# Kernel tuning notes

Measured on AMD Instinct MI355X. Metric: run time of the kernel, lower is better.

The kernel has to match this reference:

```python
import jax, jax.numpy as jnp
import numpy as np

B, S, DIN, DQK, DV = 4, 4096, 1024, 64, 64


def setup_inputs() -> dict:
    key = jax.random.key(0)
    ks = jax.random.split(key, 10)
    inv = 1.0 / np.sqrt(DIN)
    return {
        "query": jax.random.normal(ks[0], (B, S, DIN), dtype=jnp.float32),
        "key": jax.random.normal(ks[1], (B, S, DIN), dtype=jnp.float32),
        "value": jax.random.normal(ks[2], (B, S, DIN), dtype=jnp.float32),
        "mask": jnp.ones((B, S, S), dtype=jnp.int32),
        "Wq": jax.random.uniform(ks[3], (DIN, DQK), jnp.float32, -inv, inv),
        "bq": jax.random.uniform(ks[4], (DQK,), jnp.float32, -inv, inv),
        "Wk": jax.random.uniform(ks[5], (DIN, DQK), jnp.float32, -inv, inv),
        "bk": jax.random.uniform(ks[6], (DQK,), jnp.float32, -inv, inv),
        "Wv": jax.random.uniform(ks[7], (DIN, DV), jnp.float32, -inv, inv),
        "bv": jax.random.uniform(ks[8], (DV,), jnp.float32, -inv, inv),
    }


def reference(query, key, value, mask, Wq, bq, Wk, bk, Wv, bv):
    q = jnp.einsum("bsd,de->bse", query, Wq) + bq  # [B,S,DQK]
    k = jnp.einsum("bsd,de->bse", key, Wk) + bk    # [B,S,DQK]
    v = jnp.einsum("bsd,de->bse", value, Wv) + bv  # [B,S,DV]
    # faithful nonstandard scale: sqrt(dim_qk + 1e-8)
    scale = jnp.sqrt(jnp.float32(q.shape[-1]) + 1e-8)
    scores = jnp.einsum("bqe,bke->bqk", q, k) / scale  # [B,S,S]
    scores = jnp.where(mask == 0, jnp.float32(-jnp.inf), scores)
    attn = jax.nn.softmax(scores, axis=-1)
    return jnp.einsum("bqk,bkv->bqv", attn, v)  # [B,S,DV]
```

## Files before the change

kernel.cpp:

```cpp
#include <hip/hip_runtime.h>

#define NB 4
#define NS 4096
#define NDIN 1024
#define ND 64

typedef __attribute__((ext_vector_type(4))) float f32x4;
typedef __attribute__((ext_vector_type(8))) short s16x8;
typedef __attribute__((ext_vector_type(4))) short s16x4;

__device__ __forceinline__ unsigned short f2bf(float f) {
  union { float f; unsigned u; } x; x.f = f;
  unsigned r = x.u + 0x7fffu + ((x.u >> 16) & 1u);
  return (unsigned short)(r >> 16);
}

__device__ __forceinline__ unsigned cvtpk(float lo, float hi) {
  unsigned r;
  asm("v_cvt_pk_bf16_f32 %0, %1, %2" : "=v"(r) : "v"(lo), "v"(hi));
  return r;
}

__device__ __forceinline__ void gload16(const void* g, void* l) {
  __builtin_amdgcn_global_load_lds(
      (const __attribute__((address_space(1))) void*)g,
      (__attribute__((address_space(3))) void*)l, 16, 0, 0);
}

__global__ __launch_bounds__(256) void prep_w_kernel(
    const float* __restrict__ Wq, const float* __restrict__ Wk,
    const float* __restrict__ Wv, unsigned short* __restrict__ wt) {
  int idx = blockIdx.x * 256 + threadIdx.x;
  int m = idx >> 16;
  int r = idx & 65535;
  int c = r >> 10;
  int k = r & 1023;
  const float* W = (m == 0) ? Wq : (m == 1) ? Wk : Wv;
  wt[idx] = f2bf(W[k * ND + c]);
}

__global__ __launch_bounds__(256, 3) void proj_kernel(
    const float* __restrict__ Xq, const float* __restrict__ Xk, const float* __restrict__ Xv,
    const float* __restrict__ bq, const float* __restrict__ bk, const float* __restrict__ bv,
    const unsigned short* __restrict__ wt_all,
    unsigned short* __restrict__ q_o, unsigned short* __restrict__ k_o,
    unsigned short* __restrict__ vt_o) {
  __shared__ float xsm[2][4096];
  __shared__ unsigned short wsm[2][4096];

  const int y = blockIdx.y;
  const float* __restrict__ X = (y == 0) ? Xq : (y == 1) ? Xk : Xv;
  const float* __restrict__ bias = (y == 0) ? bq : (y == 1) ? bk : bv;
  const char* __restrict__ wg = (const char*)(wt_all + y * (ND * NDIN));
  const int row0 = blockIdx.x * 64;
  const int tid = threadIdx.x;
  const int lane = tid & 63;
  const int w = tid >> 6;
  const int ql = lane & 15;
  const int grp = lane >> 4;
  const int swz = (ql & 7) << 4;

  int osrcX[4];
  #pragma unroll
  for (int j = 0; j < 4; ++j) {
    const int o = w * 4096 + j * 1024 + lane * 16;
    const int row = o >> 8, c = o & 255;
    osrcX[j] = row * 4096 + (c ^ ((row & 7) << 4));
  }
  int osrcW[2];
  #pragma unroll
  for (int j = 0; j < 2; ++j) {
    const int o = w * 2048 + j * 1024 + lane * 16;
    const int row = o >> 7, c = o & 127;
    osrcW[j] = row * 2048 + (c ^ ((row & 7) << 4));
  }

  const char* xg = (const char*)(X + (size_t)row0 * NDIN);
  auto stageX = [&](int kk, int buf) {
    const char* src = xg + kk * 256;
    char* dst = (char*)xsm + buf * 16384 + w * 4096;
    #pragma unroll
    for (int j = 0; j < 4; ++j) gload16(src + osrcX[j], dst + j * 1024);
  };
  auto stageW = [&](int kk, int buf) {
    const char* src = wg + kk * 128;
    char* dst = (char*)wsm + buf * 8192 + w * 2048;
    gload16(src + osrcW[0], dst);
    gload16(src + osrcW[1], dst + 1024);
  };

  const int fw0 = (grp * 16) ^ swz;
  const int fw1 = (grp * 16 + 64) ^ swz;

  f32x4 acc[4] = {};

  stageX(0, 0);
  stageW(0, 0);
  asm volatile("s_waitcnt vmcnt(0)" ::: "memory");
  __syncthreads();

  for (int kk = 0; kk < 16; ++kk) {
    const int cur = kk & 1;
    if (kk < 15) {
      stageX(kk + 1, cur ^ 1);
      stageW(kk + 1, cur ^ 1);
    }
    __builtin_amdgcn_sched_barrier(0);

    const char* xr = (const char*)xsm + cur * 16384 + (16 * w + ql) * 256;
    const char* wr = (const char*)wsm + cur * 8192;
    #pragma unroll
    for (int half = 0; half < 2; ++half) {
      const f32x4 a0 = *reinterpret_cast<const f32x4*>(
          xr + ((half * 128 + grp * 32) ^ swz));
      const f32x4 a1 = *reinterpret_cast<const f32x4*>(
          xr + ((half * 128 + grp * 32 + 16) ^ swz));
      union { s16x8 v; unsigned u[4]; } a;
      a.u[0] = cvtpk(a0[0], a0[1]);
      a.u[1] = cvtpk(a0[2], a0[3]);
      a.u[2] = cvtpk(a1[0], a1[1]);
      a.u[3] = cvtpk(a1[2], a1[3]);
      const int fw = half ? fw1 : fw0;
      #pragma unroll
      for (int nt = 0; nt < 4; ++nt) {
        const s16x8 bfr = *reinterpret_cast<const s16x8*>(wr + (ql + 16 * nt) * 128 + fw);
        acc[nt] = __builtin_amdgcn_mfma_f32_16x16x32_bf16(a.v, bfr, acc[nt], 0, 0, 0);
      }
    }

    asm volatile("s_waitcnt vmcnt(0)" ::: "memory");
    __syncthreads();
  }

  const int b = row0 >> 12;
  const int s0 = row0 & 4095;
  #pragma unroll
  for (int nt = 0; nt < 4; ++nt) {
    const int col = ql + 16 * nt;
    const float bia = bias[col];
    #pragma unroll
    for (int r = 0; r < 4; ++r) {
      const int rr = 16 * w + grp * 4 + r;
      const unsigned short h = f2bf(acc[nt][r] + bia);
      if (y == 0) {
        q_o[(size_t)(row0 + rr) * ND + col] = h;
      } else if (y == 1) {
        k_o[(size_t)(row0 + rr) * ND + col] = h;
      } else {
        vt_o[(size_t)b * ND * NS + (size_t)col * NS + (s0 + rr)] = h;
      }
    }
  }
}

__global__ __launch_bounds__(256, 3) void attn_kernel(
    const unsigned short* __restrict__ qm, const unsigned short* __restrict__ km,
    const unsigned short* __restrict__ vt, const int* __restrict__ mask,
    float* __restrict__ opart, float* __restrict__ ml) {
  __shared__ unsigned short ksm[2][4096];
  __shared__ unsigned short vsm[2][4096];
  __shared__ unsigned short psm[4096];

  const int bid = blockIdx.x;
  const int combo = bid & 15;
  const int qblk = bid >> 4;
  const int b = combo >> 2;
  const int split = combo & 3;
  const int q0 = qblk * 64;
  const int kv00 = split * 1024;

  const int tid = threadIdx.x;
  const int lane = tid & 63;
  const int w = tid >> 6;
  const int ql = lane & 15;
  const int grp = lane >> 4;

  const int swz = (ql & 7) << 4;
  const int fK0 = ql * 128 + ((grp * 16) ^ swz);
  const int fK1 = ql * 128 + ((grp * 16 + 64) ^ swz);

  int oK0, oK1, oV0, oV1;
  {
    const int o0 = w * 2048 + lane * 16;
    const int o1 = o0 + 1024;
    oK0 = o0 ^ (((o0 >> 7) & 7) << 4);
    oK1 = o1 ^ (((o1 >> 7) & 7) << 4);
    const int d0 = o0 >> 7, c0 = o0 & 127;
    const int d1 = o1 >> 7, c1 = o1 & 127;
    oV0 = d0 * 8192 + (c0 ^ ((d0 & 7) << 4));
    oV1 = d1 * 8192 + (c1 ^ ((d1 & 7) << 4));
  }

  const char* kg = (const char*)(km + (size_t)b * NS * ND + (size_t)kv00 * ND);
  const char* vg = (const char*)(vt + (size_t)b * ND * NS + kv00);
  char* const klds = (char*)&ksm[0][0] + w * 2048;
  char* const vlds = (char*)&vsm[0][0] + w * 2048;
  char* const pw = (char*)&psm[0] + w * 2048;

  const size_t qrow = (size_t)(b * NS + q0 + w * 16 + ql) * ND;
  const s16x8 qf0 = *reinterpret_cast<const s16x8*>(qm + qrow + grp * 8);
  const s16x8 qf1 = *reinterpret_cast<const s16x8*>(qm + qrow + 32 + grp * 8);

  const int* __restrict__ mrow =
      mask + (size_t)(b * NS + q0 + w * 16 + ql) * NS + kv00;

  f32x4 acc[4] = {};
  float m_i = -INFINITY;
  float l_i = 0.f;
  const float CSC = 0.18033688011112042f;
  const float THR = 11.54f;

  auto stage = [&](int t, int buf) {
    const char* kt = kg + (size_t)t * 8192;
    const char* vtb = vg + (size_t)t * 128;
    gload16(kt + oK0, klds + buf * 8192);
    gload16(kt + oK1, klds + buf * 8192 + 1024);
    gload16(vtb + oV0, vlds + buf * 8192);
    gload16(vtb + oV1, vlds + buf * 8192 + 1024);
  };

  int4 mc[2][4];

  stage(0, 0);
  {
    mc[0][0] = *reinterpret_cast<const int4*>(mrow + grp * 4);
    mc[0][1] = *reinterpret_cast<const int4*>(mrow + 16 + grp * 4);
    mc[0][2] = *reinterpret_cast<const int4*>(mrow + 32 + grp * 4);
    mc[0][3] = *reinterpret_cast<const int4*>(mrow + 48 + grp * 4);
  }
  asm volatile("s_waitcnt vmcnt(0)" ::: "memory");
  __syncthreads();

  for (int tt = 0; tt < 16; tt += 2) {
    #pragma unroll
    for (int ph = 0; ph < 2; ++ph) {
      const int t = tt + ph;
      const int cur = ph;

      if (t < 15) {
        stage(t + 1, cur ^ 1);
        const int* mn = mrow + (t + 1) * 64;
        mc[ph ^ 1][0] = *reinterpret_cast<const int4*>(mn + grp * 4);
        mc[ph ^ 1][1] = *reinterpret_cast<const int4*>(mn + 16 + grp * 4);
        mc[ph ^ 1][2] = *reinterpret_cast<const int4*>(mn + 32 + grp * 4);
        mc[ph ^ 1][3] = *reinterpret_cast<const int4*>(mn + 48 + grp * 4);
      }
      __builtin_amdgcn_sched_barrier(0);

      const char* kread = (const char*)&ksm[0][0] + cur * 8192;
      const char* vread = (const char*)&vsm[0][0] + cur * 8192;

      f32x4 s4[4];
      __builtin_amdgcn_s_setprio(1);
      #pragma unroll
      for (int mt = 0; mt < 4; ++mt) {
        const s16x8 kf0 = *reinterpret_cast<const s16x8*>(kread + mt * 2048 + fK0);
        const s16x8 kf1 = *reinterpret_cast<const s16x8*>(kread + mt * 2048 + fK1);
        f32x4 s = {0.f, 0.f, 0.f, 0.f};
        s = __builtin_amdgcn_mfma_f32_16x16x32_bf16(kf0, qf0, s, 0, 0, 0);
        s = __builtin_amdgcn_mfma_f32_16x16x32_bf16(kf1, qf1, s, 0, 0, 0);
        s4[mt] = s;
      }
      __builtin_amdgcn_s_setprio(0);

      float sc[16];
      #pragma unroll
      for (int mt = 0; mt < 4; ++mt) {
        const int4 m = mc[ph][mt];
        sc[4 * mt + 0] = (m.x != 0) ? s4[mt][0] * CSC : -1e30f;
        sc[4 * mt + 1] = (m.y != 0) ? s4[mt][1] * CSC : -1e30f;
        sc[4 * mt + 2] = (m.z != 0) ? s4[mt][2] * CSC : -1e30f;
        sc[4 * mt + 3] = (m.w != 0) ? s4[mt][3] * CSC : -1e30f;
      }

      float t0 = fmaxf(fmaxf(sc[0], sc[1]), fmaxf(sc[2], sc[3]));
      float t1 = fmaxf(fmaxf(sc[4], sc[5]), fmaxf(sc[6], sc[7]));
      float t2 = fmaxf(fmaxf(sc[8], sc[9]), fmaxf(sc[10], sc[11]));
      float t3 = fmaxf(fmaxf(sc[12], sc[13]), fmaxf(sc[14], sc[15]));
      float tm = fmaxf(fmaxf(t0, t1), fmaxf(t2, t3));
      tm = fmaxf(tm, __shfl_xor(tm, 16));
      tm = fmaxf(tm, __shfl_xor(tm, 32));
      if (!__all(tm <= m_i + THR)) {
        const float nm = fmaxf(m_i, tm);
        const float alpha = exp2f(m_i - nm);
        #pragma unroll
        for (int r = 0; r < 4; ++r) {
          const float ar = __shfl(alpha, grp * 4 + r);
          acc[0][r] *= ar;
          acc[1][r] *= ar;
          acc[2][r] *= ar;
          acc[3][r] *= ar;
        }
        l_i *= alpha;
        m_i = nm;
      }
      #pragma unroll
      for (int r = 0; r < 16; ++r) sc[r] = exp2f(sc[r] - m_i);
      float u0 = (sc[0] + sc[1]) + (sc[2] + sc[3]);
      float u1 = (sc[4] + sc[5]) + (sc[6] + sc[7]);
      float u2 = (sc[8] + sc[9]) + (sc[10] + sc[11]);
      float u3 = (sc[12] + sc[13]) + (sc[14] + sc[15]);
      float ssum = (u0 + u1) + (u2 + u3);
      ssum += __shfl_xor(ssum, 16);
      ssum += __shfl_xor(ssum, 32);
      l_i += ssum;

      #pragma unroll
      for (int mt = 0; mt < 4; ++mt) {
        uint2 pk;
        pk.x = cvtpk(sc[4 * mt + 0], sc[4 * mt + 1]);
        pk.y = cvtpk(sc[4 * mt + 2], sc[4 * mt + 3]);
        *reinterpret_cast<uint2*>(pw + ql * 128 + ((mt * 32 + grp * 8) ^ swz)) = pk;
      }

      #pragma unroll
      for (int ks = 0; ks < 2; ++ks) {
        const s16x8 pa = *reinterpret_cast<const s16x8*>(
            pw + ql * 128 + ((ks * 64 + grp * 16) ^ swz));
        const int fV = ks ? fK1 : fK0;
        __builtin_amdgcn_s_setprio(1);
        #pragma unroll
        for (int nt = 0; nt < 4; ++nt) {
          const s16x8 vb = *reinterpret_cast<const s16x8*>(vread + nt * 2048 + fV);
          acc[nt] = __builtin_amdgcn_mfma_f32_16x16x32_bf16(pa, vb, acc[nt], 0, 0, 0);
        }
        __builtin_amdgcn_s_setprio(0);
      }

      if (t < 15) {
        asm volatile("s_waitcnt vmcnt(16)" ::: "memory");
        __syncthreads();
      }
    }
  }

  const int qg = b * NS + q0 + w * 16;
  float* obase = opart + ((size_t)split * (NB * NS) + qg) * 64;
  #pragma unroll
  for (int nt = 0; nt < 4; ++nt) {
    #pragma unroll
    for (int r = 0; r < 4; ++r) {
      obase[(size_t)(grp * 4 + r) * 64 + ql + 16 * nt] = acc[nt][r];
    }
  }
  if (grp == 0) {
    float* mlp = ml + ((size_t)split * (NB * NS) + qg + ql) * 2;
    mlp[0] = m_i;
    mlp[1] = l_i;
  }
}

__global__ __launch_bounds__(256) void combine_kernel(
    const float* __restrict__ opart, const float* __restrict__ ml,
    float* __restrict__ out) {
  const int idx = blockIdx.x * 256 + threadIdx.x;
  const int q = idx >> 4;
  const int dc = (idx & 15) * 4;
  const float2 a0 = *reinterpret_cast<const float2*>(ml + (size_t)q * 2);
  const float2 a1 = *reinterpret_cast<const float2*>(ml + (size_t)(16384 + q) * 2);
  const float2 a2 = *reinterpret_cast<const float2*>(ml + (size_t)(32768 + q) * 2);
  const float2 a3 = *reinterpret_cast<const float2*>(ml + (size_t)(49152 + q) * 2);
  const float M = fmaxf(fmaxf(a0.x, a1.x), fmaxf(a2.x, a3.x));
  const float w0 = exp2f(a0.x - M), w1 = exp2f(a1.x - M);
  const float w2 = exp2f(a2.x - M), w3 = exp2f(a3.x - M);
  const float inv = 1.f / (a0.y * w0 + a1.y * w1 + a2.y * w2 + a3.y * w3);
  f32x4 o = (*reinterpret_cast<const f32x4*>(opart + (size_t)q * 64 + dc)) * w0;
  o += (*reinterpret_cast<const f32x4*>(opart + ((size_t)16384 + q) * 64 + dc)) * w1;
  o += (*reinterpret_cast<const f32x4*>(opart + ((size_t)32768 + q) * 64 + dc)) * w2;
  o += (*reinterpret_cast<const f32x4*>(opart + ((size_t)49152 + q) * 64 + dc)) * w3;
  o *= inv;
  *reinterpret_cast<f32x4*>(out + (size_t)q * 64 + dc) = o;
}

extern "C" void kernel_launch(void* const* d_in, const int* in_sizes, int n_in,
                              void* d_out, int out_size, void* d_ws, size_t ws_size,
                              hipStream_t stream) {
  const float* query = (const float*)d_in[0];
  const float* key   = (const float*)d_in[1];
  const float* value = (const float*)d_in[2];
  const int*   mask  = (const int*)d_in[3];
  const float* Wq = (const float*)d_in[4];
  const float* bq = (const float*)d_in[5];
  const float* Wk = (const float*)d_in[6];
  const float* bk = (const float*)d_in[7];
  const float* Wv = (const float*)d_in[8];
  const float* bv = (const float*)d_in[9];
  float* out = (float*)d_out;

  char* ws = (char*)d_ws;
  unsigned short* wt    = (unsigned short*)(ws);
  unsigned short* qb    = (unsigned short*)(ws + 393216);
  unsigned short* kb    = (unsigned short*)(ws + 2490368);
  unsigned short* vtb   = (unsigned short*)(ws + 4587520);
  float*          opart = (float*)(ws + 6684672);
  float*          mlb   = (float*)(ws + 23461888);

  prep_w_kernel<<<dim3(768), dim3(256), 0, stream>>>(Wq, Wk, Wv, wt);
  proj_kernel<<<dim3(256, 3), dim3(256), 0, stream>>>(query, key, value,
                                                      bq, bk, bv, wt, qb, kb, vtb);
  attn_kernel<<<dim3(1024), dim3(256), 0, stream>>>(qb, kb, vtb, mask, opart, mlb);
  combine_kernel<<<dim3(1024), dim3(256), 0, stream>>>(opart, mlb, out);
}
```

Before: 132.0 us.

## Drop split-KV and combine kernel; one block per query tile with XCD mapping

Removes the 4-way split over the key dimension, so each block walks all 4096 keys and normalizes its output directly, which eliminates the partial-output writes and the combine kernel launch. The grid shrinks from 1024 to 256 blocks, with block ids mapped so each XCD pair handles one batch for L2 locality. Launch bounds drop to one block per SM, and the barrier becomes a raw s_barrier. The risk is much less parallelism: 256 blocks on a 256-CU part gives one wave of long-running blocks, with less latency hiding for the large mask stream.

```diff
diff --git a/kernel.cpp b/kernel.cpp
--- a/kernel.cpp
+++ b/kernel.cpp
@@ -153,21 +153,19 @@
   }
 }
 
-__global__ __launch_bounds__(256, 3) void attn_kernel(
+__global__ __launch_bounds__(256, 1) void attn_kernel(
     const unsigned short* __restrict__ qm, const unsigned short* __restrict__ km,
     const unsigned short* __restrict__ vt, const int* __restrict__ mask,
-    float* __restrict__ opart, float* __restrict__ ml) {
+    float* __restrict__ out) {
   __shared__ unsigned short ksm[2][4096];
   __shared__ unsigned short vsm[2][4096];
   __shared__ unsigned short psm[4096];
 
   const int bid = blockIdx.x;
-  const int combo = bid & 15;
-  const int qblk = bid >> 4;
-  const int b = combo >> 2;
-  const int split = combo & 3;
+  const int xcd = bid & 7;
+  const int b = xcd >> 1;
+  const int qblk = (bid >> 3) + (xcd & 1) * 32;
   const int q0 = qblk * 64;
-  const int kv00 = split * 1024;
 
   const int tid = threadIdx.x;
   const int lane = tid & 63;
@@ -191,8 +189,8 @@
     oV1 = d1 * 8192 + (c1 ^ ((d1 & 7) << 4));
   }
 
-  const char* kg = (const char*)(km + (size_t)b * NS * ND + (size_t)kv00 * ND);
-  const char* vg = (const char*)(vt + (size_t)b * ND * NS + kv00);
+  const char* kg = (const char*)(km + (size_t)b * NS * ND);
+  const char* vg = (const char*)(vt + (size_t)b * ND * NS);
   char* const klds = (char*)&ksm[0][0] + w * 2048;
   char* const vlds = (char*)&vsm[0][0] + w * 2048;
   char* const pw = (char*)&psm[0] + w * 2048;
@@ -201,8 +199,7 @@
   const s16x8 qf0 = *reinterpret_cast<const s16x8*>(qm + qrow + grp * 8);
   const s16x8 qf1 = *reinterpret_cast<const s16x8*>(qm + qrow + 32 + grp * 8);
 
-  const int* __restrict__ mrow =
-      mask + (size_t)(b * NS + q0 + w * 16 + ql) * NS + kv00;
+  const int* __restrict__ mrow = mask + (size_t)(b * NS + q0 + w * 16 + ql) * NS;
 
   f32x4 acc[4] = {};
   float m_i = -INFINITY;
@@ -231,21 +228,22 @@
   asm volatile("s_waitcnt vmcnt(0)" ::: "memory");
   __syncthreads();
 
-  for (int tt = 0; tt < 16; tt += 2) {
+  for (int tt = 0; tt < 64; tt += 2) {
     #pragma unroll
     for (int ph = 0; ph < 2; ++ph) {
       const int t = tt + ph;
       const int cur = ph;
 
-      if (t < 15) {
+      if (t < 63) {
         stage(t + 1, cur ^ 1);
+        __builtin_amdgcn_sched_barrier(0);
         const int* mn = mrow + (t + 1) * 64;
         mc[ph ^ 1][0] = *reinterpret_cast<const int4*>(mn + grp * 4);
         mc[ph ^ 1][1] = *reinterpret_cast<const int4*>(mn + 16 + grp * 4);
         mc[ph ^ 1][2] = *reinterpret_cast<const int4*>(mn + 32 + grp * 4);
         mc[ph ^ 1][3] = *reinterpret_cast<const int4*>(mn + 48 + grp * 4);
-      }
-      __builtin_amdgcn_sched_barrier(0);
+        __builtin_amdgcn_sched_barrier(0);
+      }
 
       const char* kread = (const char*)&ksm[0][0] + cur * 8192;
       const char* vread = (const char*)&vsm[0][0] + cur * 8192;
@@ -327,49 +325,23 @@
         __builtin_amdgcn_s_setprio(0);
       }
 
-      if (t < 15) {
+      if (t < 63) {
         asm volatile("s_waitcnt vmcnt(16)" ::: "memory");
-        __syncthreads();
-      }
-    }
-  }
-
-  const int qg = b * NS + q0 + w * 16;
-  float* obase = opart + ((size_t)split * (NB * NS) + qg) * 64;
+        __builtin_amdgcn_s_barrier();
+      }
+    }
+  }
+
+  const float linv = 1.f / l_i;
+  float* obase = out + ((size_t)(b * NS + q0 + w * 16)) * 64;
   #pragma unroll
-  for (int nt = 0; nt < 4; ++nt) {
-    #pragma unroll
-    for (int r = 0; r < 4; ++r) {
-      obase[(size_t)(grp * 4 + r) * 64 + ql + 16 * nt] = acc[nt][r];
-    }
-  }
-  if (grp == 0) {
-    float* mlp = ml + ((size_t)split * (NB * NS) + qg + ql) * 2;
-    mlp[0] = m_i;
-    mlp[1] = l_i;
-  }
-}
-
-__global__ __launch_bounds__(256) void combine_kernel(
-    const float* __restrict__ opart, const float* __restrict__ ml,
-    float* __restrict__ out) {
-  const int idx = blockIdx.x * 256 + threadIdx.x;
-  const int q = idx >> 4;
-  const int dc = (idx & 15) * 4;
-  const float2 a0 = *reinterpret_cast<const float2*>(ml + (size_t)q * 2);
-  const float2 a1 = *reinterpret_cast<const float2*>(ml + (size_t)(16384 + q) * 2);
-  const float2 a2 = *reinterpret_cast<const float2*>(ml + (size_t)(32768 + q) * 2);
-  const float2 a3 = *reinterpret_cast<const float2*>(ml + (size_t)(49152 + q) * 2);
-  const float M = fmaxf(fmaxf(a0.x, a1.x), fmaxf(a2.x, a3.x));
-  const float w0 = exp2f(a0.x - M), w1 = exp2f(a1.x - M);
-  const float w2 = exp2f(a2.x - M), w3 = exp2f(a3.x - M);
-  const float inv = 1.f / (a0.y * w0 + a1.y * w1 + a2.y * w2 + a3.y * w3);
-  f32x4 o = (*reinterpret_cast<const f32x4*>(opart + (size_t)q * 64 + dc)) * w0;
-  o += (*reinterpret_cast<const f32x4*>(opart + ((size_t)16384 + q) * 64 + dc)) * w1;
-  o += (*reinterpret_cast<const f32x4*>(opart + ((size_t)32768 + q) * 64 + dc)) * w2;
-  o += (*reinterpret_cast<const f32x4*>(opart + ((size_t)49152 + q) * 64 + dc)) * w3;
-  o *= inv;
-  *reinterpret_cast<f32x4*>(out + (size_t)q * 64 + dc) = o;
+  for (int r = 0; r < 4; ++r) {
+    const float ar = __shfl(linv, grp * 4 + r);
+    #pragma unroll
+    for (int nt = 0; nt < 4; ++nt) {
+      obase[(size_t)(grp * 4 + r) * 64 + ql + 16 * nt] = acc[nt][r] * ar;
+    }
+  }
 }
 
 extern "C" void kernel_launch(void* const* d_in, const int* in_sizes, int n_in,
@@ -388,16 +360,13 @@
   float* out = (float*)d_out;
 
   char* ws = (char*)d_ws;
-  unsigned short* wt    = (unsigned short*)(ws);
-  unsigned short* qb    = (unsigned short*)(ws + 393216);
-  unsigned short* kb    = (unsigned short*)(ws + 2490368);
-  unsigned short* vtb   = (unsigned short*)(ws + 4587520);
-  float*          opart = (float*)(ws + 6684672);
-  float*          mlb   = (float*)(ws + 23461888);
+  unsigned short* wt  = (unsigned short*)(ws);
+  unsigned short* qb  = (unsigned short*)(ws + 393216);
+  unsigned short* kb  = (unsigned short*)(ws + 2490368);
+  unsigned short* vtb = (unsigned short*)(ws + 4587520);
 
   prep_w_kernel<<<dim3(768), dim3(256), 0, stream>>>(Wq, Wk, Wv, wt);
   proj_kernel<<<dim3(256, 3), dim3(256), 0, stream>>>(query, key, value,
                                                       bq, bk, bv, wt, qb, kb, vtb);
-  attn_kernel<<<dim3(1024), dim3(256), 0, stream>>>(qb, kb, vtb, mask, opart, mlb);
-  combine_kernel<<<dim3(1024), dim3(256), 0, stream>>>(opart, mlb, out);
-}
+  attn_kernel<<<dim3(256), dim3(256), 0, stream>>>(qb, kb, vtb, mask, out);
+}
```

New measurement: 165.6 us. +25.4%, slower.
